# Kernel optimization log

Measured on AMD Instinct MI355X. Metric: run time of the kernel, lower is better.

The kernel has to match this reference:

```python
import jax, jax.numpy as jnp
import numpy as np

B, S, D = 16, 1024, 1024
H, HD = 16, 64  # head_dim = D // H
INIT_STD = 0.002
DEFAULT_BETA = 1.0 / np.sqrt(HD)


def setup_inputs() -> dict:
    key = jax.random.key(0)
    k1, k2, k3 = jax.random.split(key, 3)
    x = jax.random.normal(k1, (B, S, D), dtype=jnp.float32)
    q_proj_weight = jax.random.normal(k2, (H, HD, D), dtype=jnp.float32) * INIT_STD
    k_proj_weight = jax.random.normal(k3, (H, HD, D), dtype=jnp.float32) * INIT_STD
    beta = jnp.full((H,), DEFAULT_BETA, dtype=jnp.float32)
    return {"x": x, "q_proj_weight": q_proj_weight, "k_proj_weight": k_proj_weight, "beta": beta}


def reference(x, q_proj_weight, k_proj_weight, beta):
    # q, k: (B, S, H, HD)
    q = jnp.einsum('bse,hde->bshd', x, q_proj_weight)
    k = jnp.einsum('bse,hde->bshd', x, k_proj_weight)
    # scores: (B, H, S_query, S_key) with per-head beta temperature
    scores = jnp.einsum('bshd,bthd,h->bhst', q, k, beta)
    # self-attention exclusion: mask the diagonal (B == C) with -inf
    seq = scores.shape[-1]
    diag = jnp.eye(seq, dtype=bool)
    scores = jnp.where(diag[None, None], -jnp.inf, scores)
    # stable logsumexp over keys, then energy = -sum_h,s lse / beta_h
    lse = jax.nn.logsumexp(scores, axis=-1)  # (B, H, S)
    energy = -(lse / beta[None, :, None]).sum()
    return energy
```

## Files before the change

### kernel.cpp

```cpp
#include <hip/hip_runtime.h>
#include <hip/hip_bf16.h>


using short8  = __attribute__((ext_vector_type(8))) short;
using f32x4   = __attribute__((ext_vector_type(4))) float;
using ushort8 = __attribute__((ext_vector_type(8))) unsigned short;
using float4v = __attribute__((ext_vector_type(4))) float;

#define B_  16
#define S_  1024
#define D_  1024
#define H_  16
#define HD_ 64
#define LOG2E 1.4426950408889634f
#define LN2   0.6931471805599453f

#if __has_builtin(__builtin_amdgcn_exp2f)
#define EXP2F(x) __builtin_amdgcn_exp2f(x)
#else
#define EXP2F(x) exp2f(x)
#endif
#if __has_builtin(__builtin_amdgcn_logf)
#define LOG2F(x) __builtin_amdgcn_logf(x)
#else
#define LOG2F(x) log2f(x)
#endif

__device__ inline unsigned short f2bf(float f) {
  union { float f; unsigned u; } v; v.f = f;
  unsigned r = v.u + 0x7FFFu + ((v.u >> 16) & 1u);
  return (unsigned short)(r >> 16);
}

__global__ __launch_bounds__(256) void cvt_bf16_k(const float* __restrict__ in,
                                                  unsigned short* __restrict__ out, int n8) {
  int i = blockIdx.x * 256 + threadIdx.x;
  if (i >= n8) return;
  const float4v* p = (const float4v*)in;
  float4v a = p[2 * i], b = p[2 * i + 1];
  ushort8 r;
  r[0] = f2bf(a[0]); r[1] = f2bf(a[1]); r[2] = f2bf(a[2]); r[3] = f2bf(a[3]);
  r[4] = f2bf(b[0]); r[5] = f2bf(b[1]); r[6] = f2bf(b[2]); r[7] = f2bf(b[3]);
  ((ushort8*)out)[i] = r;
}

__global__ void zero_out_k(float* o) { if (threadIdx.x == 0) *o = 0.f; }

__device__ inline void gload_lds16(const void* g, void* l) {
  __builtin_amdgcn_global_load_lds((const __attribute__((address_space(1))) void*)g,
                                   (__attribute__((address_space(3))) void*)l, 16, 0, 0);
}

__device__ inline void stage_tile(const char* src, int stride, char* lds, int tid) {
  int lane = tid & 63, wave = tid >> 6;
#pragma unroll
  for (int r = 0; r < 4; ++r) {
    int o   = r * 4096 + wave * 1024 + lane * 16;
    int row = o >> 7;
    int kb  = o & 127;
    int skb = kb ^ ((row & 7) << 4);
    gload_lds16(src + (size_t)row * stride + skb, lds + (r * 4096 + wave * 1024));
  }
}

__device__ inline short8 ld_frag(const char* lds, int row, int kk, int lane) {
  int kb   = kk * 64 + ((lane >> 4) << 4);
  int addr = row * 128 + (kb ^ ((row & 7) << 4));
  return *(const short8*)(lds + addr);
}

__global__ __launch_bounds__(256) void proj_gemm_k(const unsigned short* __restrict__ Xb,
                                                   const unsigned short* __restrict__ Wqb,
                                                   const unsigned short* __restrict__ Wkb,
                                                   const float* __restrict__ beta,
                                                   unsigned short* __restrict__ Qg,
                                                   unsigned short* __restrict__ Kg) {
  __shared__ char As[16384];
  __shared__ char Bs[16384];
  const int tid = threadIdx.x, lane = tid & 63, wave = tid >> 6;
  const int wr = wave >> 1, wc = wave & 1;
  const int wgid = (blockIdx.x & 7) * 256 + (blockIdx.x >> 3);
  const int mt = wgid >> 4, nz = wgid & 15;
  const int m0 = mt * 128, n0 = (nz & 7) * 128, z = nz >> 3;
  const unsigned short* W = z ? Wkb : Wqb;
  unsigned short* Out = z ? Kg : Qg;
  const char* Abase = (const char*)Xb + (size_t)m0 * (D_ * 2);
  const char* Bbase = (const char*)W  + (size_t)n0 * (D_ * 2);

  f32x4 acc[4][4];
#pragma unroll
  for (int i = 0; i < 4; ++i)
#pragma unroll
    for (int j = 0; j < 4; ++j)
#pragma unroll
      for (int q = 0; q < 4; ++q) acc[i][j][q] = 0.f;

  for (int kt = 0; kt < D_ / 64; ++kt) {
    stage_tile(Abase + kt * 128, D_ * 2, As, tid);
    stage_tile(Bbase + kt * 128, D_ * 2, Bs, tid);
    __syncthreads();
#pragma unroll
    for (int kk = 0; kk < 2; ++kk) {
      short8 a[4], b[4];
#pragma unroll
      for (int i = 0; i < 4; ++i) a[i] = ld_frag(As, wr * 64 + i * 16 + (lane & 15), kk, lane);
#pragma unroll
      for (int i = 0; i < 4; ++i) b[i] = ld_frag(Bs, wc * 64 + i * 16 + (lane & 15), kk, lane);
#pragma unroll
      for (int i = 0; i < 4; ++i)
#pragma unroll
        for (int j = 0; j < 4; ++j)
          acc[i][j] = __builtin_amdgcn_mfma_f32_16x16x32_bf16(a[i], b[j], acc[i][j], 0, 0, 0);
    }
    __syncthreads();
  }

  const float scl = z ? 1.0f : beta[(n0 >> 6) + wc] * LOG2E;
#pragma unroll
  for (int mi = 0; mi < 4; ++mi)
#pragma unroll
    for (int ni = 0; ni < 4; ++ni)
#pragma unroll
      for (int j = 0; j < 4; ++j) {
        int m = m0 + wr * 64 + mi * 16 + ((lane >> 4) << 2) + j;
        int n = n0 + wc * 64 + ni * 16 + (lane & 15);
        int bb = m >> 10, s = m & (S_ - 1);
        int h = n >> 6, hd = n & (HD_ - 1);
        Out[(((size_t)bb * H_ + h) * S_ + s) * HD_ + hd] = f2bf(acc[mi][ni][j] * scl);
      }
}

__global__ __launch_bounds__(256) void attn_lse_k(const unsigned short* __restrict__ Qg,
                                                  const unsigned short* __restrict__ Kg,
                                                  const float* __restrict__ beta,
                                                  float* __restrict__ out) {
  __shared__ char Ks[2][16384];
  __shared__ float wsum[4];
  const int tid = threadIdx.x, lane = tid & 63, wave = tid >> 6;
  const int wgid = (blockIdx.x & 7) * 256 + (blockIdx.x >> 3);
  const int qt = wgid & 7, hb = wgid >> 3;
  const int h = hb & 15, b = hb >> 4;
  const char* qbase = (const char*)Qg + (((size_t)b * H_ + h) * S_) * (HD_ * 2);
  const char* kbase = (const char*)Kg + (((size_t)b * H_ + h) * S_) * (HD_ * 2);

  stage_tile(qbase + (size_t)qt * 16384, 128, Ks[0], tid);
  __syncthreads();
  short8 qa[2][2];
#pragma unroll
  for (int mi = 0; mi < 2; ++mi)
#pragma unroll
    for (int kk = 0; kk < 2; ++kk)
      qa[mi][kk] = ld_frag(Ks[0], wave * 32 + mi * 16 + (lane & 15), kk, lane);
  stage_tile(kbase, 128, Ks[1], tid);
  __syncthreads();

  float rs[2][4];
#pragma unroll
  for (int mi = 0; mi < 2; ++mi)
#pragma unroll
    for (int j = 0; j < 4; ++j) rs[mi][j] = 0.f;

  int cur = 1;
  for (int kt = 0; kt < 8; ++kt) {
    if (kt < 7) stage_tile(kbase + (size_t)(kt + 1) * 16384, 128, Ks[cur ^ 1], tid);

    f32x4 acc[2][8];
#pragma unroll
    for (int i = 0; i < 2; ++i)
#pragma unroll
      for (int j = 0; j < 8; ++j)
#pragma unroll
        for (int q = 0; q < 4; ++q) acc[i][j][q] = 0.f;

    __builtin_amdgcn_s_setprio(1);
#pragma unroll
    for (int kk = 0; kk < 2; ++kk)
#pragma unroll
      for (int ni = 0; ni < 8; ++ni) {
        short8 kf = ld_frag(Ks[cur], ni * 16 + (lane & 15), kk, lane);
        acc[0][ni] = __builtin_amdgcn_mfma_f32_16x16x32_bf16(qa[0][kk], kf, acc[0][ni], 0, 0, 0);
        acc[1][ni] = __builtin_amdgcn_mfma_f32_16x16x32_bf16(qa[1][kk], kf, acc[1][ni], 0, 0, 0);
      }
    __builtin_amdgcn_s_setprio(0);

    if (kt == qt) {
#pragma unroll
      for (int mi = 0; mi < 2; ++mi)
#pragma unroll
        for (int ni = 0; ni < 8; ++ni) {
          f32x4 v = acc[mi][ni];
#pragma unroll
          for (int j = 0; j < 4; ++j) {
            int row = wave * 32 + mi * 16 + ((lane >> 4) << 2) + j;
            int col = ni * 16 + (lane & 15);
            float s = (row == col) ? -1e30f : v[j];
            rs[mi][j] += EXP2F(s);
          }
        }
    } else {
#pragma unroll
      for (int mi = 0; mi < 2; ++mi)
#pragma unroll
        for (int ni = 0; ni < 8; ++ni) {
          f32x4 v = acc[mi][ni];
#pragma unroll
          for (int j = 0; j < 4; ++j) rs[mi][j] += EXP2F(v[j]);
        }
    }
    __syncthreads();
    cur ^= 1;
  }

  float local = 0.f;
#pragma unroll
  for (int mi = 0; mi < 2; ++mi)
#pragma unroll
    for (int j = 0; j < 4; ++j) {
      float v = rs[mi][j];
      v += __shfl_xor(v, 1); v += __shfl_xor(v, 2);
      v += __shfl_xor(v, 4); v += __shfl_xor(v, 8);
      local += LOG2F(v);
    }
  local += __shfl_xor(local, 16);
  local += __shfl_xor(local, 32);
  if (lane == 0) wsum[wave] = local;
  __syncthreads();
  if (tid == 0) {
    float t = wsum[0] + wsum[1] + wsum[2] + wsum[3];
    atomicAdd(out, -t * LN2 / beta[h]);
  }
}

extern "C" void kernel_launch(void* const* d_in, const int* in_sizes, int n_in,
                              void* d_out, int out_size, void* d_ws, size_t ws_size,
                              hipStream_t stream) {
  const float* x    = (const float*)d_in[0];
  const float* qw   = (const float*)d_in[1];
  const float* kw   = (const float*)d_in[2];
  const float* beta = (const float*)d_in[3];
  float* out = (float*)d_out;

  char* ws = (char*)d_ws;
  unsigned short* Xb  = (unsigned short*)(ws);
  unsigned short* Wqb = (unsigned short*)(ws + 33554432);
  unsigned short* Wkb = (unsigned short*)(ws + 35651584);
  unsigned short* Qg  = (unsigned short*)(ws + 37748736);
  unsigned short* Kg  = (unsigned short*)(ws + 71303168);

  cvt_bf16_k<<<8192, 256, 0, stream>>>(x,  Xb,  (B_ * S_ * D_) / 8);
  cvt_bf16_k<<<512,  256, 0, stream>>>(qw, Wqb, (H_ * HD_ * D_) / 8);
  cvt_bf16_k<<<512,  256, 0, stream>>>(kw, Wkb, (H_ * HD_ * D_) / 8);
  zero_out_k<<<1, 64, 0, stream>>>(out);
  proj_gemm_k<<<2048, 256, 0, stream>>>(Xb, Wqb, Wkb, beta, Qg, Kg);
  attn_lse_k<<<2048, 256, 0, stream>>>(Qg, Kg, beta, out);
}
```

Measured before the change: 253.8 us.

## Fuse Q/K projections per block and load K directly into registers

The projection GEMM now computes both the Q and K outputs in one workgroup that shares the X tile. This halves the number of X tile loads and the grid size, at the cost of double the accumulator registers and an extra LDS buffer. The attention kernel stops staging K through LDS with block barriers. Each wave instead loads K fragments straight from global memory into registers, double-buffered across 64-key blocks, which removes __syncthreads but depends on cache hits for the K reuse across waves.

```diff
diff --git a/kernel.cpp b/kernel.cpp
--- a/kernel.cpp
+++ b/kernel.cpp
@@ -76,46 +76,51 @@
                                                    unsigned short* __restrict__ Qg,
                                                    unsigned short* __restrict__ Kg) {
   __shared__ char As[16384];
-  __shared__ char Bs[16384];
+  __shared__ char Bqs[16384];
+  __shared__ char Bks[16384];
   const int tid = threadIdx.x, lane = tid & 63, wave = tid >> 6;
   const int wr = wave >> 1, wc = wave & 1;
-  const int wgid = (blockIdx.x & 7) * 256 + (blockIdx.x >> 3);
-  const int mt = wgid >> 4, nz = wgid & 15;
-  const int m0 = mt * 128, n0 = (nz & 7) * 128, z = nz >> 3;
-  const unsigned short* W = z ? Wkb : Wqb;
-  unsigned short* Out = z ? Kg : Qg;
-  const char* Abase = (const char*)Xb + (size_t)m0 * (D_ * 2);
-  const char* Bbase = (const char*)W  + (size_t)n0 * (D_ * 2);
-
-  f32x4 acc[4][4];
+  const int wgid = (blockIdx.x & 7) * 128 + (blockIdx.x >> 3);
+  const int mt = wgid >> 3, np = wgid & 7;
+  const int m0 = mt * 128, n0 = np * 128;
+  const char* Abase  = (const char*)Xb  + (size_t)m0 * (D_ * 2);
+  const char* Bqbase = (const char*)Wqb + (size_t)n0 * (D_ * 2);
+  const char* Bkbase = (const char*)Wkb + (size_t)n0 * (D_ * 2);
+
+  f32x4 accq[4][4], acck[4][4];
 #pragma unroll
   for (int i = 0; i < 4; ++i)
 #pragma unroll
     for (int j = 0; j < 4; ++j)
 #pragma unroll
-      for (int q = 0; q < 4; ++q) acc[i][j][q] = 0.f;
+      for (int q = 0; q < 4; ++q) { accq[i][j][q] = 0.f; acck[i][j][q] = 0.f; }
 
   for (int kt = 0; kt < D_ / 64; ++kt) {
-    stage_tile(Abase + kt * 128, D_ * 2, As, tid);
-    stage_tile(Bbase + kt * 128, D_ * 2, Bs, tid);
+    stage_tile(Abase  + kt * 128, D_ * 2, As,  tid);
+    stage_tile(Bqbase + kt * 128, D_ * 2, Bqs, tid);
+    stage_tile(Bkbase + kt * 128, D_ * 2, Bks, tid);
     __syncthreads();
 #pragma unroll
     for (int kk = 0; kk < 2; ++kk) {
-      short8 a[4], b[4];
+      short8 a[4];
 #pragma unroll
       for (int i = 0; i < 4; ++i) a[i] = ld_frag(As, wr * 64 + i * 16 + (lane & 15), kk, lane);
 #pragma unroll
-      for (int i = 0; i < 4; ++i) b[i] = ld_frag(Bs, wc * 64 + i * 16 + (lane & 15), kk, lane);
-#pragma unroll
-      for (int i = 0; i < 4; ++i)
-#pragma unroll
-        for (int j = 0; j < 4; ++j)
-          acc[i][j] = __builtin_amdgcn_mfma_f32_16x16x32_bf16(a[i], b[j], acc[i][j], 0, 0, 0);
+      for (int j = 0; j < 4; ++j) {
+        short8 bq = ld_frag(Bqs, wc * 64 + j * 16 + (lane & 15), kk, lane);
+#pragma unroll
+        for (int i = 0; i < 4; ++i)
+          accq[i][j] = __builtin_amdgcn_mfma_f32_16x16x32_bf16(a[i], bq, accq[i][j], 0, 0, 0);
+        short8 bk = ld_frag(Bks, wc * 64 + j * 16 + (lane & 15), kk, lane);
+#pragma unroll
+        for (int i = 0; i < 4; ++i)
+          acck[i][j] = __builtin_amdgcn_mfma_f32_16x16x32_bf16(a[i], bk, acck[i][j], 0, 0, 0);
+      }
     }
     __syncthreads();
   }
 
-  const float scl = z ? 1.0f : beta[(n0 >> 6) + wc] * LOG2E;
+  const float scl = beta[np * 2 + wc] * LOG2E;
 #pragma unroll
   for (int mi = 0; mi < 4; ++mi)
 #pragma unroll
@@ -126,15 +131,66 @@
         int n = n0 + wc * 64 + ni * 16 + (lane & 15);
         int bb = m >> 10, s = m & (S_ - 1);
         int h = n >> 6, hd = n & (HD_ - 1);
-        Out[(((size_t)bb * H_ + h) * S_ + s) * HD_ + hd] = f2bf(acc[mi][ni][j] * scl);
-      }
+        size_t o = (((size_t)bb * H_ + h) * S_ + s) * HD_ + hd;
+        Qg[o] = f2bf(accq[mi][ni][j] * scl);
+        Kg[o] = f2bf(acck[mi][ni][j]);
+      }
+}
+
+__device__ inline void attn_loadk(short8 (&kf)[2][4], const char* kbase, int tb, int lane) {
+#pragma unroll
+  for (int kk = 0; kk < 2; ++kk)
+#pragma unroll
+    for (int nj = 0; nj < 4; ++nj)
+      kf[kk][nj] = *(const short8*)(kbase +
+          (size_t)((tb * 64 + nj * 16 + (lane & 15)) * 128 + kk * 64 + ((lane >> 4) << 4)));
+}
+
+__device__ inline void attn_step(const short8 (&qa)[2][2], const short8 (&kf)[2][4],
+                                 float (&rs)[2][4], int tb, int dgtb, int q0w, int lane) {
+  f32x4 acc[2][4];
+#pragma unroll
+  for (int mi = 0; mi < 2; ++mi)
+#pragma unroll
+    for (int nj = 0; nj < 4; ++nj)
+#pragma unroll
+      for (int q = 0; q < 4; ++q) acc[mi][nj][q] = 0.f;
+#pragma unroll
+  for (int kk = 0; kk < 2; ++kk)
+#pragma unroll
+    for (int nj = 0; nj < 4; ++nj) {
+      acc[0][nj] = __builtin_amdgcn_mfma_f32_16x16x32_bf16(qa[0][kk], kf[kk][nj], acc[0][nj], 0, 0, 0);
+      acc[1][nj] = __builtin_amdgcn_mfma_f32_16x16x32_bf16(qa[1][kk], kf[kk][nj], acc[1][nj], 0, 0, 0);
+    }
+  if (tb == dgtb) {
+#pragma unroll
+    for (int mi = 0; mi < 2; ++mi)
+#pragma unroll
+      for (int nj = 0; nj < 4; ++nj) {
+        f32x4 v = acc[mi][nj];
+#pragma unroll
+        for (int j = 0; j < 4; ++j) {
+          int q = q0w + mi * 16 + ((lane >> 4) << 2) + j;
+          int t = tb * 64 + nj * 16 + (lane & 15);
+          rs[mi][j] += EXP2F(q == t ? -1e30f : v[j]);
+        }
+      }
+  } else {
+#pragma unroll
+    for (int mi = 0; mi < 2; ++mi)
+#pragma unroll
+      for (int nj = 0; nj < 4; ++nj) {
+        f32x4 v = acc[mi][nj];
+#pragma unroll
+        for (int j = 0; j < 4; ++j) rs[mi][j] += EXP2F(v[j]);
+      }
+  }
 }
 
 __global__ __launch_bounds__(256) void attn_lse_k(const unsigned short* __restrict__ Qg,
                                                   const unsigned short* __restrict__ Kg,
                                                   const float* __restrict__ beta,
                                                   float* __restrict__ out) {
-  __shared__ char Ks[2][16384];
   __shared__ float wsum[4];
   const int tid = threadIdx.x, lane = tid & 63, wave = tid >> 6;
   const int wgid = (blockIdx.x & 7) * 256 + (blockIdx.x >> 3);
@@ -142,17 +198,16 @@
   const int h = hb & 15, b = hb >> 4;
   const char* qbase = (const char*)Qg + (((size_t)b * H_ + h) * S_) * (HD_ * 2);
   const char* kbase = (const char*)Kg + (((size_t)b * H_ + h) * S_) * (HD_ * 2);
-
-  stage_tile(qbase + (size_t)qt * 16384, 128, Ks[0], tid);
-  __syncthreads();
+  const int q0w = qt * 128 + wave * 32;
+  const int dgtb = q0w >> 6;
+
   short8 qa[2][2];
 #pragma unroll
   for (int mi = 0; mi < 2; ++mi)
 #pragma unroll
     for (int kk = 0; kk < 2; ++kk)
-      qa[mi][kk] = ld_frag(Ks[0], wave * 32 + mi * 16 + (lane & 15), kk, lane);
-  stage_tile(kbase, 128, Ks[1], tid);
-  __syncthreads();
+      qa[mi][kk] = *(const short8*)(qbase +
+          (size_t)((q0w + mi * 16 + (lane & 15)) * 128 + kk * 64 + ((lane >> 4) << 4)));
 
   float rs[2][4];
 #pragma unroll
@@ -160,55 +215,17 @@
 #pragma unroll
     for (int j = 0; j < 4; ++j) rs[mi][j] = 0.f;
 
-  int cur = 1;
-  for (int kt = 0; kt < 8; ++kt) {
-    if (kt < 7) stage_tile(kbase + (size_t)(kt + 1) * 16384, 128, Ks[cur ^ 1], tid);
-
-    f32x4 acc[2][8];
-#pragma unroll
-    for (int i = 0; i < 2; ++i)
-#pragma unroll
-      for (int j = 0; j < 8; ++j)
-#pragma unroll
-        for (int q = 0; q < 4; ++q) acc[i][j][q] = 0.f;
-
-    __builtin_amdgcn_s_setprio(1);
-#pragma unroll
-    for (int kk = 0; kk < 2; ++kk)
-#pragma unroll
-      for (int ni = 0; ni < 8; ++ni) {
-        short8 kf = ld_frag(Ks[cur], ni * 16 + (lane & 15), kk, lane);
-        acc[0][ni] = __builtin_amdgcn_mfma_f32_16x16x32_bf16(qa[0][kk], kf, acc[0][ni], 0, 0, 0);
-        acc[1][ni] = __builtin_amdgcn_mfma_f32_16x16x32_bf16(qa[1][kk], kf, acc[1][ni], 0, 0, 0);
-      }
-    __builtin_amdgcn_s_setprio(0);
-
-    if (kt == qt) {
-#pragma unroll
-      for (int mi = 0; mi < 2; ++mi)
-#pragma unroll
-        for (int ni = 0; ni < 8; ++ni) {
-          f32x4 v = acc[mi][ni];
-#pragma unroll
-          for (int j = 0; j < 4; ++j) {
-            int row = wave * 32 + mi * 16 + ((lane >> 4) << 2) + j;
-            int col = ni * 16 + (lane & 15);
-            float s = (row == col) ? -1e30f : v[j];
-            rs[mi][j] += EXP2F(s);
-          }
-        }
+  short8 kfA[2][4], kfB[2][4];
+  attn_loadk(kfA, kbase, 0, lane);
+#pragma unroll
+  for (int tb = 0; tb < 16; ++tb) {
+    if ((tb & 1) == 0) {
+      if (tb < 15) attn_loadk(kfB, kbase, tb + 1, lane);
+      attn_step(qa, kfA, rs, tb, dgtb, q0w, lane);
     } else {
-#pragma unroll
-      for (int mi = 0; mi < 2; ++mi)
-#pragma unroll
-        for (int ni = 0; ni < 8; ++ni) {
-          f32x4 v = acc[mi][ni];
-#pragma unroll
-          for (int j = 0; j < 4; ++j) rs[mi][j] += EXP2F(v[j]);
-        }
-    }
-    __syncthreads();
-    cur ^= 1;
+      if (tb < 15) attn_loadk(kfA, kbase, tb + 1, lane);
+      attn_step(qa, kfB, rs, tb, dgtb, q0w, lane);
+    }
   }
 
   float local = 0.f;
@@ -251,6 +268,6 @@
   cvt_bf16_k<<<512,  256, 0, stream>>>(qw, Wqb, (H_ * HD_ * D_) / 8);
   cvt_bf16_k<<<512,  256, 0, stream>>>(kw, Wkb, (H_ * HD_ * D_) / 8);
   zero_out_k<<<1, 64, 0, stream>>>(out);
-  proj_gemm_k<<<2048, 256, 0, stream>>>(Xb, Wqb, Wkb, beta, Qg, Kg);
+  proj_gemm_k<<<1024, 256, 0, stream>>>(Xb, Wqb, Wkb, beta, Qg, Kg);
   attn_lse_k<<<2048, 256, 0, stream>>>(Qg, Kg, beta, out);
 }
```

After: 351.8 us. +38.6%, slower.
